# Kernel tuning notes

Hardware: AMD Instinct MI355X
Metric: run time of the kernel (lower is better)

Reference implementation:

```python
import jax, jax.numpy as jnp
import numpy as np

B, S, P, D = 32, 512, 512, 768

def setup_inputs() -> dict:
    key = jax.random.key(0)
    k1, k2 = jax.random.split(key)
    inputs = jax.random.normal(k1, (B, S, D), dtype=jnp.float32)
    prototypes = jax.random.normal(k2, (P, D), dtype=jnp.float32)
    return {"inputs": inputs, "prototypes": prototypes}

def reference(inputs, prototypes):
    # Squared Euclidean distance from every token vector to every prototype:
    # but the cross term is a GEMM and the huge [B,S,P,D] intermediate is never built).
    x_sq = jnp.sum(inputs * inputs, axis=-1, keepdims=True)          # [B, S, 1]
    p_sq = jnp.sum(prototypes * prototypes, axis=-1)                 # [P]
    cross = jnp.einsum('bsd,pd->bsp', inputs, prototypes)            # [B, S, P]
    distances = x_sq + p_sq[None, None, :] - 2.0 * cross             # [B, S, P]
    return (distances, prototypes)
```

## Files before the change

kernel.cpp:

```cpp
#include <hip/hip_runtime.h>
#include <hip/hip_bf16.h>


#define M_TOK 16384
#define N_PROT 512
#define K_DIM 768
#define BKC 128
#define NKC (K_DIM / BKC)
#define NSK (K_DIM / 32)
#define ASTR 136

typedef __attribute__((ext_vector_type(4))) float f32x4;
typedef __attribute__((ext_vector_type(8))) short bf16x8;

__device__ inline unsigned short f2bf(float f) {
    unsigned int u = __float_as_uint(f);
    u += 0x7fffu + ((u >> 16) & 1u);
    return (unsigned short)(u >> 16);
}

__global__ __launch_bounds__(256) void prep_b(
    const float* __restrict__ p,
    unsigned short* __restrict__ b_bf, float* __restrict__ p_sq,
    float* __restrict__ proto_out)
{
    const int row  = blockIdx.x * 4 + (threadIdx.x >> 6);
    const int lane = threadIdx.x & 63;

    const float4* src4 = (const float4*)(p + (size_t)row * K_DIM);
    unsigned short* dst = b_bf + (size_t)row * K_DIM;
    float4* pout4 = (float4*)(proto_out + (size_t)row * K_DIM);

    float ssum = 0.0f;
#pragma unroll
    for (int j = 0; j < 3; ++j) {
        const int idx = lane + j * 64;
        float4 v = src4[idx];
        ssum += v.x * v.x + v.y * v.y + v.z * v.z + v.w * v.w;
        ushort4 b;
        b.x = f2bf(v.x); b.y = f2bf(v.y); b.z = f2bf(v.z); b.w = f2bf(v.w);
        ((ushort4*)dst)[idx] = b;
        pout4[idx] = v;
    }
#pragma unroll
    for (int off = 32; off > 0; off >>= 1) ssum += __shfl_down(ssum, off);
    if (lane == 0) p_sq[row] = ssum;
}

__global__ __launch_bounds__(512, 4) void dist_main(
    const float* __restrict__ X,
    const unsigned short* __restrict__ Bb,
    const float* __restrict__ p_sq,
    float* __restrict__ out)
{
    __shared__ unsigned short lds_a[2][64 * ASTR];
    __shared__ float lds_xsq[64];

    const int bid     = blockIdx.x;
    const int logical = (bid & 7) * 64 + (bid >> 3);
    const int ms = logical >> 1;
    const int nh = logical & 1;
    const int bm = ms << 6;
    const int bn = nh << 8;

    const int tid  = threadIdx.x;
    const int wave = tid >> 6;
    const int lane = tid & 63;
    const int wn   = bn + (wave << 5);
    const int quad = lane >> 4;
    const int l16  = lane & 15;

    const int ar = tid >> 3;
    const int ac = tid & 7;
    const float* aptr = X + (size_t)(bm + ar) * K_DIM + ac * 4;

    float asq = 0.0f;

    {
        float4 v0 = *(const float4*)(aptr);
        float4 v1 = *(const float4*)(aptr + 32);
        float4 v2 = *(const float4*)(aptr + 64);
        float4 v3 = *(const float4*)(aptr + 96);
        float4 vv[4] = {v0, v1, v2, v3};
#pragma unroll
        for (int j = 0; j < 4; ++j) {
            float4 v = vv[j];
            asq += v.x * v.x + v.y * v.y + v.z * v.z + v.w * v.w;
            ushort4 u;
            u.x = f2bf(v.x); u.y = f2bf(v.y); u.z = f2bf(v.z); u.w = f2bf(v.w);
            *(ushort4*)&lds_a[0][ar * ASTR + (ac + 8 * j) * 4] = u;
        }
    }
    __syncthreads();

    const unsigned short* pb = Bb + (size_t)(wn + l16) * K_DIM + quad * 8;

    bf16x8 A0[2], A1[2], A2[2];
    A0[0] = *(const bf16x8*)(pb);
    A0[1] = *(const bf16x8*)(pb + 16 * K_DIM);
    A1[0] = *(const bf16x8*)(pb + 32);
    A1[1] = *(const bf16x8*)(pb + 16 * K_DIM + 32);

    const f32x4 zero = {0.0f, 0.0f, 0.0f, 0.0f};
    f32x4 acc[2][4];
#pragma unroll
    for (int pt = 0; pt < 2; ++pt)
#pragma unroll
        for (int tt = 0; tt < 4; ++tt) acc[pt][tt] = zero;

    for (int kc = 0; kc < NKC; ++kc) {
        float4 s0, s1, s2, s3;
        if (kc + 1 < NKC) {
            const float* ap = aptr + (kc + 1) * BKC;
            s0 = *(const float4*)(ap);
            s1 = *(const float4*)(ap + 32);
            s2 = *(const float4*)(ap + 64);
            s3 = *(const float4*)(ap + 96);
        }

#pragma unroll
        for (int s = 0; s < 4; ++s) {
            const int kk = kc * 4 + s;
            if (kk + 2 < NSK) {
                const int kn = (kk + 2) * 32;
                A2[0] = *(const bf16x8*)(pb + kn);
                A2[1] = *(const bf16x8*)(pb + 16 * K_DIM + kn);
            }

            bf16x8 tf[4];
#pragma unroll
            for (int tt = 0; tt < 4; ++tt)
                tf[tt] = *(const bf16x8*)&lds_a[kc & 1]
                    [(tt * 16 + l16) * ASTR + s * 32 + quad * 8];

#pragma unroll
            for (int tt = 0; tt < 4; ++tt) {
                acc[0][tt] = __builtin_amdgcn_mfma_f32_16x16x32_bf16(
                    A0[0], tf[tt], acc[0][tt], 0, 0, 0);
                acc[1][tt] = __builtin_amdgcn_mfma_f32_16x16x32_bf16(
                    A0[1], tf[tt], acc[1][tt], 0, 0, 0);
            }
            A0[0] = A1[0]; A0[1] = A1[1];
            A1[0] = A2[0]; A1[1] = A2[1];
        }

        if (kc + 1 < NKC) {
            unsigned short* aw = &lds_a[(kc + 1) & 1][ar * ASTR + ac * 4];
            float4 vv[4] = {s0, s1, s2, s3};
#pragma unroll
            for (int j = 0; j < 4; ++j) {
                float4 v = vv[j];
                asq += v.x * v.x + v.y * v.y + v.z * v.z + v.w * v.w;
                ushort4 u;
                u.x = f2bf(v.x); u.y = f2bf(v.y); u.z = f2bf(v.z); u.w = f2bf(v.w);
                *(ushort4*)(aw + 8 * j * 4) = u;
            }
        }
        __syncthreads();
    }

#pragma unroll
    for (int off = 1; off < 8; off <<= 1) asq += __shfl_xor(asq, off);
    if (ac == 0) lds_xsq[ar] = asq;
    __syncthreads();

    float4 ps4[2];
    ps4[0] = *(const float4*)&p_sq[wn + quad * 4];
    ps4[1] = *(const float4*)&p_sq[wn + 16 + quad * 4];

#pragma unroll
    for (int tt = 0; tt < 4; ++tt) {
        const float xs = lds_xsq[tt * 16 + l16];
        float* orow = out + (size_t)(bm + tt * 16 + l16) * N_PROT + wn + quad * 4;
        float4 o0, o1;
        o0.x = xs + ps4[0].x - 2.0f * acc[0][tt][0];
        o0.y = xs + ps4[0].y - 2.0f * acc[0][tt][1];
        o0.z = xs + ps4[0].z - 2.0f * acc[0][tt][2];
        o0.w = xs + ps4[0].w - 2.0f * acc[0][tt][3];
        o1.x = xs + ps4[1].x - 2.0f * acc[1][tt][0];
        o1.y = xs + ps4[1].y - 2.0f * acc[1][tt][1];
        o1.z = xs + ps4[1].z - 2.0f * acc[1][tt][2];
        o1.w = xs + ps4[1].w - 2.0f * acc[1][tt][3];
        *(float4*)(orow)      = o0;
        *(float4*)(orow + 16) = o1;
    }
}

extern "C" void kernel_launch(void* const* d_in, const int* in_sizes, int n_in,
                              void* d_out, int out_size, void* d_ws, size_t ws_size,
                              hipStream_t stream) {
    const float* inputs = (const float*)d_in[0];
    const float* protos = (const float*)d_in[1];
    float* out = (float*)d_out;
    float* proto_out = out + (size_t)M_TOK * N_PROT;

    char* ws = (char*)d_ws;
    unsigned short* b_bf = (unsigned short*)ws;
    float* p_sq = (float*)(ws + 786432);

    prep_b<<<128, 256, 0, stream>>>(protos, b_bf, p_sq, proto_out);
    dist_main<<<2 * (M_TOK / 64), 512, 0, stream>>>(inputs, b_bf, p_sq, out);
}
```

Before: 124.7 us.

## Split prototype dimension into quarters with 256-thread blocks

Each block now covers a 64x128 output tile with 4 waves instead of 64x256 with 8 waves. This doubles the grid to 1024 blocks, and the A-tile load is reworked so each thread converts eight float4s per K chunk. The aim is better occupancy and load balance across CUs. The cost is that each token tile is loaded, converted to bf16 and reduced for its squared norm four times instead of twice, doubling global reads of the input. The block remap keeps blocks that share a token tile on the same XCD so those repeat reads can hit L2.

```diff
diff --git a/kernel.cpp b/kernel.cpp
--- a/kernel.cpp
+++ b/kernel.cpp
@@ -47,7 +47,7 @@
     if (lane == 0) p_sq[row] = ssum;
 }
 
-__global__ __launch_bounds__(512, 4) void dist_main(
+__global__ __launch_bounds__(256, 4) void dist_main(
     const float* __restrict__ X,
     const unsigned short* __restrict__ Bb,
     const float* __restrict__ p_sq,
@@ -57,11 +57,11 @@
     __shared__ float lds_xsq[64];
 
     const int bid     = blockIdx.x;
-    const int logical = (bid & 7) * 64 + (bid >> 3);
-    const int ms = logical >> 1;
-    const int nh = logical & 1;
+    const int logical = (bid & 7) * 128 + (bid >> 3);
+    const int ms = logical >> 2;
+    const int nq = logical & 3;
     const int bm = ms << 6;
-    const int bn = nh << 8;
+    const int bn = nq << 7;
 
     const int tid  = threadIdx.x;
     const int wave = tid >> 6;
@@ -70,25 +70,20 @@
     const int quad = lane >> 4;
     const int l16  = lane & 15;
 
-    const int ar = tid >> 3;
-    const int ac = tid & 7;
+    const int ar = tid >> 2;
+    const int ac = tid & 3;
     const float* aptr = X + (size_t)(bm + ar) * K_DIM + ac * 4;
 
     float asq = 0.0f;
 
     {
-        float4 v0 = *(const float4*)(aptr);
-        float4 v1 = *(const float4*)(aptr + 32);
-        float4 v2 = *(const float4*)(aptr + 64);
-        float4 v3 = *(const float4*)(aptr + 96);
-        float4 vv[4] = {v0, v1, v2, v3};
 #pragma unroll
-        for (int j = 0; j < 4; ++j) {
-            float4 v = vv[j];
+        for (int j = 0; j < 8; ++j) {
+            float4 v = *(const float4*)(aptr + 16 * j);
             asq += v.x * v.x + v.y * v.y + v.z * v.z + v.w * v.w;
             ushort4 u;
             u.x = f2bf(v.x); u.y = f2bf(v.y); u.z = f2bf(v.z); u.w = f2bf(v.w);
-            *(ushort4*)&lds_a[0][ar * ASTR + (ac + 8 * j) * 4] = u;
+            *(ushort4*)&lds_a[0][ar * ASTR + (ac + 4 * j) * 4] = u;
         }
     }
     __syncthreads();
@@ -109,18 +104,16 @@
         for (int tt = 0; tt < 4; ++tt) acc[pt][tt] = zero;
 
     for (int kc = 0; kc < NKC; ++kc) {
-        float4 s0, s1, s2, s3;
+        float4 s[8];
         if (kc + 1 < NKC) {
             const float* ap = aptr + (kc + 1) * BKC;
-            s0 = *(const float4*)(ap);
-            s1 = *(const float4*)(ap + 32);
-            s2 = *(const float4*)(ap + 64);
-            s3 = *(const float4*)(ap + 96);
+#pragma unroll
+            for (int j = 0; j < 8; ++j) s[j] = *(const float4*)(ap + 16 * j);
         }
 
 #pragma unroll
-        for (int s = 0; s < 4; ++s) {
-            const int kk = kc * 4 + s;
+        for (int ss = 0; ss < 4; ++ss) {
+            const int kk = kc * 4 + ss;
             if (kk + 2 < NSK) {
                 const int kn = (kk + 2) * 32;
                 A2[0] = *(const bf16x8*)(pb + kn);
@@ -131,7 +124,7 @@
 #pragma unroll
             for (int tt = 0; tt < 4; ++tt)
                 tf[tt] = *(const bf16x8*)&lds_a[kc & 1]
-                    [(tt * 16 + l16) * ASTR + s * 32 + quad * 8];
+                    [(tt * 16 + l16) * ASTR + ss * 32 + quad * 8];
 
 #pragma unroll
             for (int tt = 0; tt < 4; ++tt) {
@@ -146,21 +139,20 @@
 
         if (kc + 1 < NKC) {
             unsigned short* aw = &lds_a[(kc + 1) & 1][ar * ASTR + ac * 4];
-            float4 vv[4] = {s0, s1, s2, s3};
 #pragma unroll
-            for (int j = 0; j < 4; ++j) {
-                float4 v = vv[j];
+            for (int j = 0; j < 8; ++j) {
+                float4 v = s[j];
                 asq += v.x * v.x + v.y * v.y + v.z * v.z + v.w * v.w;
                 ushort4 u;
                 u.x = f2bf(v.x); u.y = f2bf(v.y); u.z = f2bf(v.z); u.w = f2bf(v.w);
-                *(ushort4*)(aw + 8 * j * 4) = u;
+                *(ushort4*)(aw + 4 * j * 4) = u;
             }
         }
         __syncthreads();
     }
 
 #pragma unroll
-    for (int off = 1; off < 8; off <<= 1) asq += __shfl_xor(asq, off);
+    for (int off = 1; off < 4; off <<= 1) asq += __shfl_xor(asq, off);
     if (ac == 0) lds_xsq[ar] = asq;
     __syncthreads();
 
@@ -199,5 +191,5 @@
     float* p_sq = (float*)(ws + 786432);
 
     prep_b<<<128, 256, 0, stream>>>(protos, b_bf, p_sq, proto_out);
-    dist_main<<<2 * (M_TOK / 64), 512, 0, stream>>>(inputs, b_bf, p_sq, out);
+    dist_main<<<1024, 256, 0, stream>>>(inputs, b_bf, p_sq, out);
 }
```

After: 134.8 us. +8.1%, slower.
